# Optimization experiments

Hardware: AMD Instinct MI355X
Metric: run time of the kernel (lower is better)

Reference implementation:

```python
import jax, jax.numpy as jnp
import numpy as np

N = 100_000          # number of nodes
E = 3_200_000        # number of edges (avg degree 32)
IN_CH = 128
OUT_CH = 128


def setup_inputs() -> dict:
    key = jax.random.key(0)
    k1, k2, k3, k4 = jax.random.split(key, 4)
    x = jax.random.normal(k1, (N, IN_CH), dtype=jnp.float32)
    edge_index = jax.random.randint(k2, (2, E), 0, N, dtype=jnp.int32)
    # torch nn.Linear weights have shape [out_features, in_features]
    W_theta = jax.random.normal(k3, (OUT_CH, IN_CH), dtype=jnp.float32) / np.sqrt(IN_CH).astype(np.float32)
    W_phi = jax.random.normal(k4, (OUT_CH, OUT_CH), dtype=jnp.float32) / np.sqrt(OUT_CH).astype(np.float32)
    return {"x": x, "edge_index": edge_index, "W_theta": W_theta, "W_phi": W_phi}


def reference(x, edge_index, W_theta, W_phi):
    row, col = edge_index[0], edge_index[1]
    rel_pos = x[row] - x[col]                       # [E, in]
    rel_t = rel_pos @ W_theta.T                     # [E, out]
    aggr = jax.ops.segment_max(rel_t, row, num_segments=N)  # [N, out], -inf for empty segments
    # torch_scatter.scatter_max leaves empty segments at 0
    aggr = jnp.where(jnp.isneginf(aggr), jnp.zeros((), dtype=aggr.dtype), aggr)
    return aggr @ W_phi.T                           # [N, out]
```

## Files before the change

### kernel.cpp

```cpp
#include <hip/hip_runtime.h>
#include <stdint.h>

#define N_NODES 100000
#define N_EDGES 3200000
#define CH 128
#define NBUK 391
#define CAP 8704
#define SPLITB 782
#define EPB 4096
#define ROWS_A 50048

typedef __bf16 bf16x8 __attribute__((ext_vector_type(8)));
typedef float  floatx4 __attribute__((ext_vector_type(4)));

__device__ __forceinline__ unsigned short f2bf_bits(float f) {
    unsigned u = __float_as_uint(f);
    u += 0x7FFFu + ((u >> 16) & 1u);
    return (unsigned short)(u >> 16);
}

__device__ __forceinline__ unsigned short enc16(unsigned short b) {
    return b ^ ((b & 0x8000u) ? 0xFFFFu : 0x8000u);
}

__device__ __forceinline__ unsigned pkminu(unsigned a, unsigned b) {
    unsigned d;
    asm("v_pk_min_u16 %0, %1, %2" : "=v"(d) : "v"(a), "v"(b));
    return d;
}

__device__ __forceinline__ unsigned dec2(unsigned k) {
    unsigned lo = k & 0xFFFFu;
    unsigned hi = k >> 16;
    lo ^= (lo & 0x8000u) ? 0x8000u : 0xFFFFu;
    hi ^= (hi & 0x8000u) ? 0x8000u : 0xFFFFu;
    return lo | (hi << 16);
}

__device__ __forceinline__ bf16x8 pack8(floatx4 f0, floatx4 f1) {
    bf16x8 r;
    r[0] = (__bf16)f0[0]; r[1] = (__bf16)f0[1]; r[2] = (__bf16)f0[2]; r[3] = (__bf16)f0[3];
    r[4] = (__bf16)f1[0]; r[5] = (__bf16)f1[1]; r[6] = (__bf16)f1[2]; r[7] = (__bf16)f1[3];
    return r;
}

__device__ __forceinline__ void gemm_tile(int row0, int lane, const float* __restrict__ x,
                                          const unsigned short* __restrict__ wb,
                                          unsigned short* __restrict__ yt) {
    int m = lane & 15, quad = lane >> 4;
    bf16x8 a[4];
    const floatx4* xp = (const floatx4*)(x + (size_t)(row0 + m) * CH + quad * 8);
#pragma unroll
    for (int ks = 0; ks < 4; ks++) a[ks] = pack8(xp[ks * 8], xp[ks * 8 + 1]);

    for (int nt = 0; nt < 8; nt++) {
        const bf16x8* wp = (const bf16x8*)(wb + (size_t)(nt * 16 + m) * CH + quad * 8);
        floatx4 acc = {0.f, 0.f, 0.f, 0.f};
#pragma unroll
        for (int ks = 0; ks < 4; ks++)
            acc = __builtin_amdgcn_mfma_f32_16x16x32_bf16(a[ks], wp[ks * 4], acc, 0, 0, 0);
#pragma unroll
        for (int r = 0; r < 4; r++) {
            int orow = row0 + quad * 4 + r;
            yt[(size_t)orow * CH + nt * 16 + m] = enc16(f2bf_bits(acc[r]));
        }
    }
}

__global__ void k_setup(const float* __restrict__ Wt, const float* __restrict__ Wp,
                        unsigned short* __restrict__ wb, int* __restrict__ cursor) {
    int bid = blockIdx.x, t = threadIdx.x;
    if (bid < 128) {
        int i = bid * 256 + t;
        float v = (i < 16384) ? Wt[i] : Wp[i - 16384];
        wb[i] = f2bf_bits(v);
    } else {
        for (int i = t; i < NBUK; i += 256) cursor[i] = i * CAP;
    }
}

__global__ void k_split_gemmyA(const int* __restrict__ row, const int* __restrict__ col,
                               int* __restrict__ cursor, unsigned* __restrict__ pairs,
                               const float* __restrict__ x,
                               const unsigned short* __restrict__ wb,
                               unsigned short* __restrict__ yt) {
    __shared__ unsigned lpair[EPB];
    __shared__ int h[NBUK];
    __shared__ int hb[NBUK];
    __shared__ int lbase[NBUK];
    __shared__ int cur[NBUK];
    __shared__ int sc[512];
    int bid = blockIdx.x, t = threadIdx.x;
    if (bid < SPLITB) {
        for (int i = t; i < NBUK; i += 256) h[i] = 0;
        __syncthreads();
        int e0 = bid * EPB;
        int4 r[4];
        bool v[4];
#pragma unroll
        for (int j = 0; j < 4; j++) {
            int idx = e0 + j * 1024 + t * 4;
            v[j] = idx < N_EDGES;
            if (v[j]) {
                r[j] = *(const int4*)(row + idx);
                atomicAdd(&h[r[j].x >> 8], 1);
                atomicAdd(&h[r[j].y >> 8], 1);
                atomicAdd(&h[r[j].z >> 8], 1);
                atomicAdd(&h[r[j].w >> 8], 1);
            }
        }
        __syncthreads();
        for (int i = t; i < NBUK; i += 256) {
            int c = h[i];
            hb[i] = c ? atomicAdd(&cursor[i], c) : 0;
        }
        sc[t] = h[t];
        sc[t + 256] = (t + 256 < NBUK) ? h[t + 256] : 0;
        __syncthreads();
        for (int off = 1; off < 512; off <<= 1) {
            int a0 = (t >= off) ? sc[t - off] : 0;
            int a1 = (t + 256 >= off) ? sc[t + 256 - off] : 0;
            __syncthreads();
            sc[t] += a0;
            sc[t + 256] += a1;
            __syncthreads();
        }
        for (int i = t; i < NBUK; i += 256) {
            int lb = sc[i] - h[i];
            lbase[i] = lb;
            cur[i] = lb;
        }
        __syncthreads();
#pragma unroll
        for (int j = 0; j < 4; j++) {
            if (v[j]) {
                int idx = e0 + j * 1024 + t * 4;
                int4 c = *(const int4*)(col + idx);
                int b, p;
                b = r[j].x >> 8; p = atomicAdd(&cur[b], 1);
                lpair[p] = ((unsigned)(r[j].x & 255) << 17) | (unsigned)c.x;
                b = r[j].y >> 8; p = atomicAdd(&cur[b], 1);
                lpair[p] = ((unsigned)(r[j].y & 255) << 17) | (unsigned)c.y;
                b = r[j].z >> 8; p = atomicAdd(&cur[b], 1);
                lpair[p] = ((unsigned)(r[j].z & 255) << 17) | (unsigned)c.z;
                b = r[j].w >> 8; p = atomicAdd(&cur[b], 1);
                lpair[p] = ((unsigned)(r[j].w & 255) << 17) | (unsigned)c.w;
            }
        }
        __syncthreads();
        for (int b = t; b < NBUK; b += 256) {
            int n = h[b];
            if (!n) continue;
            int src = lbase[b];
            int dst = hb[b];
            int lim = (b + 1) * CAP - dst;
            if (n > lim) n = lim;
            for (int k = 0; k < n; k++) pairs[dst + k] = lpair[src + k];
        }
    } else {
        int wave = (bid - SPLITB) * 4 + (t >> 6);
        int row0 = wave * 16;
        if (row0 >= ROWS_A) return;
        gemm_tile(row0, t & 63, x, wb, yt);
    }
}

__global__ void k_build_gemmyB(unsigned* __restrict__ pairs, const int* __restrict__ cursor,
                               int* __restrict__ deg, int* __restrict__ offs,
                               const float* __restrict__ x,
                               const unsigned short* __restrict__ wb,
                               unsigned short* __restrict__ yt) {
    __shared__ int hist[256];
    __shared__ int sc[256];
    __shared__ int cur[256];
    __shared__ int lcsr[CAP];
    int bid = blockIdx.x, t = threadIdx.x;
    if (bid < NBUK) {
        int b = bid;
        int s0 = b * CAP;
        int cnt = cursor[b] - s0;
        if (cnt > CAP) cnt = CAP;
        if (t < 256) hist[t] = 0;
        __syncthreads();
        for (int i = t; i < cnt; i += 1024) {
            unsigned p = pairs[s0 + i];
            atomicAdd(&hist[p >> 17], 1);
        }
        __syncthreads();
        int d = 0;
        if (t < 256) { d = hist[t]; sc[t] = d; }
        __syncthreads();
        for (int off = 1; off < 256; off <<= 1) {
            int vv = 0;
            if (t < 256 && t >= off) vv = sc[t - off];
            __syncthreads();
            if (t < 256) sc[t] += vv;
            __syncthreads();
        }
        if (t < 256) {
            int excl = sc[t] - d;
            int node = b * 256 + t;
            if (node < N_NODES) {
                deg[node] = d;
                offs[node] = s0 + excl;
            }
            cur[t] = excl;
        }
        __syncthreads();
        for (int i = t; i < cnt; i += 1024) {
            unsigned p = pairs[s0 + i];
            int pos = atomicAdd(&cur[p >> 17], 1);
            lcsr[pos] = (int)(p & 0x1FFFFu);
        }
        __syncthreads();
        int* csr = (int*)pairs;
        for (int i = t; i < cnt; i += 1024) csr[s0 + i] = lcsr[i];
    } else {
        int wg = (bid - NBUK) * 16 + (t >> 6);
        int row0 = ROWS_A + wg * 16;
        if (row0 >= N_NODES) return;
        gemm_tile(row0, t & 63, x, wb, yt);
    }
}

#define PKA(v)                        \
    do {                              \
        m0 = pkminu(m0, (v).x);       \
        m1 = pkminu(m1, (v).y);       \
        m2 = pkminu(m2, (v).z);       \
        m3 = pkminu(m3, (v).w);       \
    } while (0)

__global__ void k_minaggr_out(const uint4* __restrict__ yt, const int* __restrict__ offs,
                              const int* __restrict__ deg, const int* __restrict__ csr,
                              const unsigned short* __restrict__ wb,
                              float* __restrict__ out) {
    __shared__ unsigned short atile[16 * 136];
    int t = threadIdx.x;
    int wave = t >> 6, lane = t & 63;
    int q = lane >> 4, s = lane & 15;
    int nl = wave * 4 + q;
    int n = blockIdx.x * 16 + nl;

    int i = offs[n];
    int len = deg[n];
    int end = i + len;

    unsigned m0 = ~0u, m1 = ~0u, m2 = ~0u, m3 = ~0u;

    for (; i + 8 <= end; i += 8) {
        int c0 = csr[i + 0];
        int c1 = csr[i + 1];
        int c2 = csr[i + 2];
        int c3 = csr[i + 3];
        int c4 = csr[i + 4];
        int c5 = csr[i + 5];
        int c6 = csr[i + 6];
        int c7 = csr[i + 7];
        uint4 v0 = yt[(size_t)c0 * 16 + s];
        uint4 v1 = yt[(size_t)c1 * 16 + s];
        uint4 v2 = yt[(size_t)c2 * 16 + s];
        uint4 v3 = yt[(size_t)c3 * 16 + s];
        uint4 v4 = yt[(size_t)c4 * 16 + s];
        uint4 v5 = yt[(size_t)c5 * 16 + s];
        uint4 v6 = yt[(size_t)c6 * 16 + s];
        uint4 v7 = yt[(size_t)c7 * 16 + s];
        PKA(v0); PKA(v1); PKA(v2); PKA(v3);
        PKA(v4); PKA(v5); PKA(v6); PKA(v7);
    }
    for (; i < end; i++) {
        int c = csr[i];
        uint4 v = yt[(size_t)c * 16 + s];
        PKA(v);
    }

    uint4 outv = {0u, 0u, 0u, 0u};
    if (len > 0) {
        unsigned d0 = dec2(m0), d1 = dec2(m1), d2 = dec2(m2), d3 = dec2(m3);
        uint4 se = yt[(size_t)n * 16 + s];
        unsigned s0 = dec2(se.x), s1 = dec2(se.y), s2 = dec2(se.z), s3 = dec2(se.w);
        outv.x = (unsigned)f2bf_bits(__uint_as_float(s0 << 16) - __uint_as_float(d0 << 16)) |
                 ((unsigned)f2bf_bits(__uint_as_float(s0 & 0xFFFF0000u) -
                                      __uint_as_float(d0 & 0xFFFF0000u)) << 16);
        outv.y = (unsigned)f2bf_bits(__uint_as_float(s1 << 16) - __uint_as_float(d1 << 16)) |
                 ((unsigned)f2bf_bits(__uint_as_float(s1 & 0xFFFF0000u) -
                                      __uint_as_float(d1 & 0xFFFF0000u)) << 16);
        outv.z = (unsigned)f2bf_bits(__uint_as_float(s2 << 16) - __uint_as_float(d2 << 16)) |
                 ((unsigned)f2bf_bits(__uint_as_float(s2 & 0xFFFF0000u) -
                                      __uint_as_float(d2 & 0xFFFF0000u)) << 16);
        outv.w = (unsigned)f2bf_bits(__uint_as_float(s3 << 16) - __uint_as_float(d3 << 16)) |
                 ((unsigned)f2bf_bits(__uint_as_float(s3 & 0xFFFF0000u) -
                                      __uint_as_float(d3 & 0xFFFF0000u)) << 16);
    }
    *(uint4*)&atile[nl * 136 + s * 8] = outv;
    __syncthreads();

    int m = lane & 15, quad = lane >> 4;
    bf16x8 a[4];
#pragma unroll
    for (int ks = 0; ks < 4; ks++)
        a[ks] = *(const bf16x8*)&atile[m * 136 + ks * 32 + quad * 8];

#pragma unroll
    for (int ntl = 0; ntl < 2; ntl++) {
        int nt = wave * 2 + ntl;
        const bf16x8* wp = (const bf16x8*)(wb + (size_t)(nt * 16 + m) * CH + quad * 8);
        floatx4 acc = {0.f, 0.f, 0.f, 0.f};
#pragma unroll
        for (int ks = 0; ks < 4; ks++)
            acc = __builtin_amdgcn_mfma_f32_16x16x32_bf16(a[ks], wp[ks * 4], acc, 0, 0, 0);
#pragma unroll
        for (int r = 0; r < 4; r++)
            out[(size_t)(blockIdx.x * 16 + quad * 4 + r) * CH + nt * 16 + m] = acc[r];
    }
}

extern "C" void kernel_launch(void* const* d_in, const int* in_sizes, int n_in,
                              void* d_out, int out_size, void* d_ws, size_t ws_size,
                              hipStream_t stream) {
    const float* x   = (const float*)d_in[0];
    const int* edge  = (const int*)d_in[1];
    const float* Wt  = (const float*)d_in[2];
    const float* Wp  = (const float*)d_in[3];
    const int* row = edge;
    const int* col = edge + N_EDGES;
    float* out = (float*)d_out;

    char* ws = (char*)d_ws;
    int* deg    = (int*)ws;  ws += 400128;
    int* offs   = (int*)ws;  ws += 400128;
    int* cursor = (int*)ws;  ws += 2048;
    unsigned short* yt = (unsigned short*)ws; ws += 25600000;
    unsigned short* wb = (unsigned short*)ws; ws += 65536;
    unsigned* pairs = (unsigned*)ws; ws += (size_t)NBUK * CAP * 4;

    k_setup<<<129, 256, 0, stream>>>(Wt, Wp, wb, cursor);
    k_split_gemmyA<<<SPLITB + 782, 256, 0, stream>>>(row, col, cursor, pairs,
                                                     x, wb, yt);
    k_build_gemmyB<<<NBUK + 196, 1024, 0, stream>>>(pairs, cursor, deg, offs, x, wb, yt);
    k_minaggr_out<<<N_NODES / 16, 256, 0, stream>>>((const uint4*)yt, offs, deg,
                                                    (const int*)pairs, wb + 16384, out);
}
```

Before: 296.1 us.

## Replace atomic bucket cursors with deterministic histogram-scan-scatter and spread GEMM over stages

Bucket partitioning now runs in three kernels instead of one fused split kernel with global atomics. A per-block histogram is written out, a per-bucket scan across blocks computes deterministic base offsets, and a scatter pass re-reads row and col to place the pairs. The dense x·Wθ GEMM tiles are spread evenly across the four pre-aggregation kernels so they fill the otherwise light stages. This removes the global atomic contention on cursor and makes bucket ordering deterministic, at the cost of an extra launch, a second read of row, and about 2.4 MB of counts/bases traffic.

```diff
diff --git a/kernel.cpp b/kernel.cpp
--- a/kernel.cpp
+++ b/kernel.cpp
@@ -8,7 +8,6 @@
 #define CAP 8704
 #define SPLITB 782
 #define EPB 4096
-#define ROWS_A 50048
 
 typedef __bf16 bf16x8 __attribute__((ext_vector_type(8)));
 typedef float  floatx4 __attribute__((ext_vector_type(4)));
@@ -68,22 +67,93 @@
 }
 
 __global__ void k_setup(const float* __restrict__ Wt, const float* __restrict__ Wp,
-                        unsigned short* __restrict__ wb, int* __restrict__ cursor) {
+                        unsigned short* __restrict__ wb) {
+    int i = blockIdx.x * 256 + threadIdx.x;
+    float v = (i < 16384) ? Wt[i] : Wp[i - 16384];
+    wb[i] = f2bf_bits(v);
+}
+
+__global__ void k_hist_gemmy(const int* __restrict__ row, int* __restrict__ counts,
+                             const float* __restrict__ x,
+                             const unsigned short* __restrict__ wb,
+                             unsigned short* __restrict__ yt) {
+    __shared__ int h[NBUK];
     int bid = blockIdx.x, t = threadIdx.x;
-    if (bid < 128) {
-        int i = bid * 256 + t;
-        float v = (i < 16384) ? Wt[i] : Wp[i - 16384];
-        wb[i] = f2bf_bits(v);
+    if (bid < SPLITB) {
+        for (int i = t; i < NBUK; i += 256) h[i] = 0;
+        __syncthreads();
+        int e0 = bid * EPB;
+#pragma unroll
+        for (int j = 0; j < 4; j++) {
+            int idx = e0 + j * 1024 + t * 4;
+            if (idx < N_EDGES) {
+                int4 r = *(const int4*)(row + idx);
+                atomicAdd(&h[r.x >> 8], 1);
+                atomicAdd(&h[r.y >> 8], 1);
+                atomicAdd(&h[r.z >> 8], 1);
+                atomicAdd(&h[r.w >> 8], 1);
+            }
+        }
+        __syncthreads();
+        for (int i = t; i < NBUK; i += 256) counts[bid * NBUK + i] = h[i];
     } else {
-        for (int i = t; i < NBUK; i += 256) cursor[i] = i * CAP;
-    }
-}
-
-__global__ void k_split_gemmyA(const int* __restrict__ row, const int* __restrict__ col,
-                               int* __restrict__ cursor, unsigned* __restrict__ pairs,
-                               const float* __restrict__ x,
-                               const unsigned short* __restrict__ wb,
-                               unsigned short* __restrict__ yt) {
+        int wave = (bid - SPLITB) * 4 + (t >> 6);
+        int row0 = wave * 16;
+        if (row0 >= 25024) return;
+        gemm_tile(row0, t & 63, x, wb, yt);
+    }
+}
+
+__global__ void k_scan_gemmy(const int* __restrict__ counts, int* __restrict__ bases,
+                             int* __restrict__ bcnt,
+                             const float* __restrict__ x,
+                             const unsigned short* __restrict__ wb,
+                             unsigned short* __restrict__ yt) {
+    __shared__ int sc[256];
+    int bid = blockIdx.x, t = threadIdx.x;
+    if (bid < NBUK) {
+        int b = bid;
+        int v[4];
+        int s = 0;
+#pragma unroll
+        for (int k = 0; k < 4; k++) {
+            int blk = t * 4 + k;
+            v[k] = (blk < SPLITB) ? counts[blk * NBUK + b] : 0;
+            s += v[k];
+        }
+        sc[t] = s;
+        __syncthreads();
+        for (int off = 1; off < 256; off <<= 1) {
+            int a = (t >= off) ? sc[t - off] : 0;
+            __syncthreads();
+            sc[t] += a;
+            __syncthreads();
+        }
+        int incl = sc[t];
+        int run = incl - s;
+#pragma unroll
+        for (int k = 0; k < 4; k++) {
+            int blk = t * 4 + k;
+            if (blk < SPLITB) {
+                bases[blk * NBUK + b] = b * CAP + run;
+                run += v[k];
+            }
+        }
+        if (t == 255) bcnt[b] = incl;
+    } else {
+        int wave = (bid - NBUK) * 4 + (t >> 6);
+        int row0 = 25024 + wave * 16;
+        if (row0 >= 50048) return;
+        gemm_tile(row0, t & 63, x, wb, yt);
+    }
+}
+
+__global__ void k_scatter_gemmy(const int* __restrict__ row, const int* __restrict__ col,
+                                const int* __restrict__ counts, const int* __restrict__ bases,
+                                unsigned* __restrict__ pairs,
+                                const float* __restrict__ x,
+                                const unsigned short* __restrict__ wb,
+                                unsigned short* __restrict__ yt) {
     __shared__ unsigned lpair[EPB];
     __shared__ int h[NBUK];
     __shared__ int hb[NBUK];
@@ -92,27 +162,9 @@
     __shared__ int sc[512];
     int bid = blockIdx.x, t = threadIdx.x;
     if (bid < SPLITB) {
-        for (int i = t; i < NBUK; i += 256) h[i] = 0;
-        __syncthreads();
-        int e0 = bid * EPB;
-        int4 r[4];
-        bool v[4];
-#pragma unroll
-        for (int j = 0; j < 4; j++) {
-            int idx = e0 + j * 1024 + t * 4;
-            v[j] = idx < N_EDGES;
-            if (v[j]) {
-                r[j] = *(const int4*)(row + idx);
-                atomicAdd(&h[r[j].x >> 8], 1);
-                atomicAdd(&h[r[j].y >> 8], 1);
-                atomicAdd(&h[r[j].z >> 8], 1);
-                atomicAdd(&h[r[j].w >> 8], 1);
-            }
-        }
-        __syncthreads();
         for (int i = t; i < NBUK; i += 256) {
-            int c = h[i];
-            hb[i] = c ? atomicAdd(&cursor[i], c) : 0;
+            h[i] = counts[bid * NBUK + i];
+            hb[i] = bases[bid * NBUK + i];
         }
         sc[t] = h[t];
         sc[t + 256] = (t + 256 < NBUK) ? h[t + 256] : 0;
@@ -131,20 +183,22 @@
             cur[i] = lb;
         }
         __syncthreads();
+        int e0 = bid * EPB;
 #pragma unroll
         for (int j = 0; j < 4; j++) {
-            if (v[j]) {
-                int idx = e0 + j * 1024 + t * 4;
+            int idx = e0 + j * 1024 + t * 4;
+            if (idx < N_EDGES) {
+                int4 r = *(const int4*)(row + idx);
                 int4 c = *(const int4*)(col + idx);
                 int b, p;
-                b = r[j].x >> 8; p = atomicAdd(&cur[b], 1);
-                lpair[p] = ((unsigned)(r[j].x & 255) << 17) | (unsigned)c.x;
-                b = r[j].y >> 8; p = atomicAdd(&cur[b], 1);
-                lpair[p] = ((unsigned)(r[j].y & 255) << 17) | (unsigned)c.y;
-                b = r[j].z >> 8; p = atomicAdd(&cur[b], 1);
-                lpair[p] = ((unsigned)(r[j].z & 255) << 17) | (unsigned)c.z;
-                b = r[j].w >> 8; p = atomicAdd(&cur[b], 1);
-                lpair[p] = ((unsigned)(r[j].w & 255) << 17) | (unsigned)c.w;
+                b = r.x >> 8; p = atomicAdd(&cur[b], 1);
+                lpair[p] = ((unsigned)(r.x & 255) << 17) | (unsigned)c.x;
+                b = r.y >> 8; p = atomicAdd(&cur[b], 1);
+                lpair[p] = ((unsigned)(r.y & 255) << 17) | (unsigned)c.y;
+                b = r.z >> 8; p = atomicAdd(&cur[b], 1);
+                lpair[p] = ((unsigned)(r.z & 255) << 17) | (unsigned)c.z;
+                b = r.w >> 8; p = atomicAdd(&cur[b], 1);
+                lpair[p] = ((unsigned)(r.w & 255) << 17) | (unsigned)c.w;
             }
         }
         __syncthreads();
@@ -159,17 +213,17 @@
         }
     } else {
         int wave = (bid - SPLITB) * 4 + (t >> 6);
-        int row0 = wave * 16;
-        if (row0 >= ROWS_A) return;
+        int row0 = 50048 + wave * 16;
+        if (row0 >= 75072) return;
         gemm_tile(row0, t & 63, x, wb, yt);
     }
 }
 
-__global__ void k_build_gemmyB(unsigned* __restrict__ pairs, const int* __restrict__ cursor,
-                               int* __restrict__ deg, int* __restrict__ offs,
-                               const float* __restrict__ x,
-                               const unsigned short* __restrict__ wb,
-                               unsigned short* __restrict__ yt) {
+__global__ void k_build_gemmy(unsigned* __restrict__ pairs, const int* __restrict__ bcnt,
+                              int* __restrict__ deg, int* __restrict__ offs,
+                              const float* __restrict__ x,
+                              const unsigned short* __restrict__ wb,
+                              unsigned short* __restrict__ yt) {
     __shared__ int hist[256];
     __shared__ int sc[256];
     __shared__ int cur[256];
@@ -178,7 +232,7 @@
     if (bid < NBUK) {
         int b = bid;
         int s0 = b * CAP;
-        int cnt = cursor[b] - s0;
+        int cnt = bcnt[b];
         if (cnt > CAP) cnt = CAP;
         if (t < 256) hist[t] = 0;
         __syncthreads();
@@ -217,7 +271,7 @@
         for (int i = t; i < cnt; i += 1024) csr[s0 + i] = lcsr[i];
     } else {
         int wg = (bid - NBUK) * 16 + (t >> 6);
-        int row0 = ROWS_A + wg * 16;
+        int row0 = 75072 + wg * 16;
         if (row0 >= N_NODES) return;
         gemm_tile(row0, t & 63, x, wb, yt);
     }
@@ -329,15 +383,19 @@
     char* ws = (char*)d_ws;
     int* deg    = (int*)ws;  ws += 400128;
     int* offs   = (int*)ws;  ws += 400128;
-    int* cursor = (int*)ws;  ws += 2048;
+    int* bcnt   = (int*)ws;  ws += 2048;
+    int* counts = (int*)ws;  ws += 1223168;
+    int* bases  = (int*)ws;  ws += 1223168;
     unsigned short* yt = (unsigned short*)ws; ws += 25600000;
     unsigned short* wb = (unsigned short*)ws; ws += 65536;
     unsigned* pairs = (unsigned*)ws; ws += (size_t)NBUK * CAP * 4;
 
-    k_setup<<<129, 256, 0, stream>>>(Wt, Wp, wb, cursor);
-    k_split_gemmyA<<<SPLITB + 782, 256, 0, stream>>>(row, col, cursor, pairs,
-                                                     x, wb, yt);
-    k_build_gemmyB<<<NBUK + 196, 1024, 0, stream>>>(pairs, cursor, deg, offs, x, wb, yt);
+    k_setup<<<128, 256, 0, stream>>>(Wt, Wp, wb);
+    k_hist_gemmy<<<SPLITB + 391, 256, 0, stream>>>(row, counts, x, wb, yt);
+    k_scan_gemmy<<<NBUK + 391, 256, 0, stream>>>(counts, bases, bcnt, x, wb, yt);
+    k_scatter_gemmy<<<SPLITB + 391, 256, 0, stream>>>(row, col, counts, bases, pairs,
+                                                      x, wb, yt);
+    k_build_gemmy<<<NBUK + 98, 1024, 0, stream>>>(pairs, bcnt, deg, offs, x, wb, yt);
     k_minaggr_out<<<N_NODES / 16, 256, 0, stream>>>((const uint4*)yt, offs, deg,
                                                     (const int*)pairs, wb + 16384, out);
 }
```

Result: no change. 294.2 us (-0.6%).

## Split yt into two channel banks and gather-min each half in separate kernels

Applied to the files above, without the earlier changes.

Stores the projected node features as two 64-channel banks instead of one 128-channel row layout. The min-aggregation then runs as two passes, each gathering only one bank, so each pass has a 12.8 MB working set that may stay resident in cache. The first half-result goes through an intermediate buffer, and the second kernel adds the output GEMM over 32 nodes per block. The cost is an extra launch, a second read of the CSR indices, and an extra write and read of the intermediate buffer.

```diff
diff --git a/kernel.cpp b/kernel.cpp
--- a/kernel.cpp
+++ b/kernel.cpp
@@ -9,6 +9,7 @@
 #define SPLITB 782
 #define EPB 4096
 #define ROWS_A 50048
+#define BANK_U4 800000
 
 typedef __bf16 bf16x8 __attribute__((ext_vector_type(8)));
 typedef float  floatx4 __attribute__((ext_vector_type(4)));
@@ -62,7 +63,8 @@
 #pragma unroll
         for (int r = 0; r < 4; r++) {
             int orow = row0 + quad * 4 + r;
-            yt[(size_t)orow * CH + nt * 16 + m] = enc16(f2bf_bits(acc[r]));
+            yt[(size_t)(nt >> 2) * (N_NODES * 64) + (size_t)orow * 64 + (nt & 3) * 16 + m] =
+                enc16(f2bf_bits(acc[r]));
         }
     }
 }
@@ -231,79 +233,118 @@
         m3 = pkminu(m3, (v).w);       \
     } while (0)
 
-__global__ void k_minaggr_out(const uint4* __restrict__ yt, const int* __restrict__ offs,
-                              const int* __restrict__ deg, const int* __restrict__ csr,
-                              const unsigned short* __restrict__ wb,
-                              float* __restrict__ out) {
-    __shared__ unsigned short atile[16 * 136];
+__device__ __forceinline__ uint4 finish_half(unsigned m0, unsigned m1, unsigned m2, unsigned m3,
+                                             uint4 se) {
+    unsigned d0 = dec2(m0), d1 = dec2(m1), d2 = dec2(m2), d3 = dec2(m3);
+    unsigned s0 = dec2(se.x), s1 = dec2(se.y), s2 = dec2(se.z), s3 = dec2(se.w);
+    uint4 o;
+    o.x = (unsigned)f2bf_bits(__uint_as_float(s0 << 16) - __uint_as_float(d0 << 16)) |
+          ((unsigned)f2bf_bits(__uint_as_float(s0 & 0xFFFF0000u) -
+                               __uint_as_float(d0 & 0xFFFF0000u)) << 16);
+    o.y = (unsigned)f2bf_bits(__uint_as_float(s1 << 16) - __uint_as_float(d1 << 16)) |
+          ((unsigned)f2bf_bits(__uint_as_float(s1 & 0xFFFF0000u) -
+                               __uint_as_float(d1 & 0xFFFF0000u)) << 16);
+    o.z = (unsigned)f2bf_bits(__uint_as_float(s2 << 16) - __uint_as_float(d2 << 16)) |
+          ((unsigned)f2bf_bits(__uint_as_float(s2 & 0xFFFF0000u) -
+                               __uint_as_float(d2 & 0xFFFF0000u)) << 16);
+    o.w = (unsigned)f2bf_bits(__uint_as_float(s3 << 16) - __uint_as_float(d3 << 16)) |
+          ((unsigned)f2bf_bits(__uint_as_float(s3 & 0xFFFF0000u) -
+                               __uint_as_float(d3 & 0xFFFF0000u)) << 16);
+    return o;
+}
+
+__global__ void k_min0(const uint4* __restrict__ yt, const int* __restrict__ offs,
+                       const int* __restrict__ deg, const int* __restrict__ csr,
+                       uint4* __restrict__ mbuf) {
     int t = threadIdx.x;
-    int wave = t >> 6, lane = t & 63;
-    int q = lane >> 4, s = lane & 15;
-    int nl = wave * 4 + q;
-    int n = blockIdx.x * 16 + nl;
+    int lane = t & 63;
+    int nl = (t >> 6) * 8 + (lane >> 3);
+    int s8 = lane & 7;
+    int n = blockIdx.x * 32 + nl;
 
     int i = offs[n];
     int len = deg[n];
     int end = i + len;
-
     unsigned m0 = ~0u, m1 = ~0u, m2 = ~0u, m3 = ~0u;
 
     for (; i + 8 <= end; i += 8) {
-        int c0 = csr[i + 0];
-        int c1 = csr[i + 1];
-        int c2 = csr[i + 2];
-        int c3 = csr[i + 3];
-        int c4 = csr[i + 4];
-        int c5 = csr[i + 5];
-        int c6 = csr[i + 6];
-        int c7 = csr[i + 7];
-        uint4 v0 = yt[(size_t)c0 * 16 + s];
-        uint4 v1 = yt[(size_t)c1 * 16 + s];
-        uint4 v2 = yt[(size_t)c2 * 16 + s];
-        uint4 v3 = yt[(size_t)c3 * 16 + s];
-        uint4 v4 = yt[(size_t)c4 * 16 + s];
-        uint4 v5 = yt[(size_t)c5 * 16 + s];
-        uint4 v6 = yt[(size_t)c6 * 16 + s];
-        uint4 v7 = yt[(size_t)c7 * 16 + s];
+        int c0 = csr[i + 0], c1 = csr[i + 1], c2 = csr[i + 2], c3 = csr[i + 3];
+        int c4 = csr[i + 4], c5 = csr[i + 5], c6 = csr[i + 6], c7 = csr[i + 7];
+        uint4 v0 = yt[(size_t)c0 * 8 + s8];
+        uint4 v1 = yt[(size_t)c1 * 8 + s8];
+        uint4 v2 = yt[(size_t)c2 * 8 + s8];
+        uint4 v3 = yt[(size_t)c3 * 8 + s8];
+        uint4 v4 = yt[(size_t)c4 * 8 + s8];
+        uint4 v5 = yt[(size_t)c5 * 8 + s8];
+        uint4 v6 = yt[(size_t)c6 * 8 + s8];
+        uint4 v7 = yt[(size_t)c7 * 8 + s8];
         PKA(v0); PKA(v1); PKA(v2); PKA(v3);
         PKA(v4); PKA(v5); PKA(v6); PKA(v7);
     }
     for (; i < end; i++) {
-        int c = csr[i];
-        uint4 v = yt[(size_t)c * 16 + s];
+        uint4 v = yt[(size_t)csr[i] * 8 + s8];
         PKA(v);
     }
 
     uint4 outv = {0u, 0u, 0u, 0u};
-    if (len > 0) {
-        unsigned d0 = dec2(m0), d1 = dec2(m1), d2 = dec2(m2), d3 = dec2(m3);
-        uint4 se = yt[(size_t)n * 16 + s];
-        unsigned s0 = dec2(se.x), s1 = dec2(se.y), s2 = dec2(se.z), s3 = dec2(se.w);
-        outv.x = (unsigned)f2bf_bits(__uint_as_float(s0 << 16) - __uint_as_float(d0 << 16)) |
-                 ((unsigned)f2bf_bits(__uint_as_float(s0 & 0xFFFF0000u) -
-                                      __uint_as_float(d0 & 0xFFFF0000u)) << 16);
-        outv.y = (unsigned)f2bf_bits(__uint_as_float(s1 << 16) - __uint_as_float(d1 << 16)) |
-                 ((unsigned)f2bf_bits(__uint_as_float(s1 & 0xFFFF0000u) -
-                                      __uint_as_float(d1 & 0xFFFF0000u)) << 16);
-        outv.z = (unsigned)f2bf_bits(__uint_as_float(s2 << 16) - __uint_as_float(d2 << 16)) |
-                 ((unsigned)f2bf_bits(__uint_as_float(s2 & 0xFFFF0000u) -
-                                      __uint_as_float(d2 & 0xFFFF0000u)) << 16);
-        outv.w = (unsigned)f2bf_bits(__uint_as_float(s3 << 16) - __uint_as_float(d3 << 16)) |
-                 ((unsigned)f2bf_bits(__uint_as_float(s3 & 0xFFFF0000u) -
-                                      __uint_as_float(d3 & 0xFFFF0000u)) << 16);
-    }
-    *(uint4*)&atile[nl * 136 + s * 8] = outv;
+    if (len > 0) outv = finish_half(m0, m1, m2, m3, yt[(size_t)n * 8 + s8]);
+    mbuf[(size_t)n * 8 + s8] = outv;
+}
+
+__global__ void k_min1_out(const uint4* __restrict__ yt, const int* __restrict__ offs,
+                           const int* __restrict__ deg, const int* __restrict__ csr,
+                           const uint4* __restrict__ mbuf,
+                           const unsigned short* __restrict__ wb,
+                           float* __restrict__ out) {
+    __shared__ unsigned short atile[32 * 136];
+    int t = threadIdx.x;
+    int wave = t >> 6, lane = t & 63;
+    int nl = wave * 8 + (lane >> 3);
+    int s8 = lane & 7;
+    int n = blockIdx.x * 32 + nl;
+    const uint4* yt1 = yt + BANK_U4;
+
+    int i = offs[n];
+    int len = deg[n];
+    int end = i + len;
+    unsigned m0 = ~0u, m1 = ~0u, m2 = ~0u, m3 = ~0u;
+
+    for (; i + 8 <= end; i += 8) {
+        int c0 = csr[i + 0], c1 = csr[i + 1], c2 = csr[i + 2], c3 = csr[i + 3];
+        int c4 = csr[i + 4], c5 = csr[i + 5], c6 = csr[i + 6], c7 = csr[i + 7];
+        uint4 v0 = yt1[(size_t)c0 * 8 + s8];
+        uint4 v1 = yt1[(size_t)c1 * 8 + s8];
+        uint4 v2 = yt1[(size_t)c2 * 8 + s8];
+        uint4 v3 = yt1[(size_t)c3 * 8 + s8];
+        uint4 v4 = yt1[(size_t)c4 * 8 + s8];
+        uint4 v5 = yt1[(size_t)c5 * 8 + s8];
+        uint4 v6 = yt1[(size_t)c6 * 8 + s8];
+        uint4 v7 = yt1[(size_t)c7 * 8 + s8];
+        PKA(v0); PKA(v1); PKA(v2); PKA(v3);
+        PKA(v4); PKA(v5); PKA(v6); PKA(v7);
+    }
+    for (; i < end; i++) {
+        uint4 v = yt1[(size_t)csr[i] * 8 + s8];
+        PKA(v);
+    }
+
+    uint4 outv = {0u, 0u, 0u, 0u};
+    if (len > 0) outv = finish_half(m0, m1, m2, m3, yt1[(size_t)n * 8 + s8]);
+    *(uint4*)&atile[nl * 136 + 64 + s8 * 8] = outv;
+    *(uint4*)&atile[nl * 136 + s8 * 8] = mbuf[(size_t)n * 8 + s8];
     __syncthreads();
 
     int m = lane & 15, quad = lane >> 4;
+    int mt = wave & 1;
+    int ng = wave >> 1;
     bf16x8 a[4];
 #pragma unroll
     for (int ks = 0; ks < 4; ks++)
-        a[ks] = *(const bf16x8*)&atile[m * 136 + ks * 32 + quad * 8];
-
-#pragma unroll
-    for (int ntl = 0; ntl < 2; ntl++) {
-        int nt = wave * 2 + ntl;
+        a[ks] = *(const bf16x8*)&atile[(mt * 16 + m) * 136 + ks * 32 + quad * 8];
+
+#pragma unroll
+    for (int ntl = 0; ntl < 4; ntl++) {
+        int nt = ng * 4 + ntl;
         const bf16x8* wp = (const bf16x8*)(wb + (size_t)(nt * 16 + m) * CH + quad * 8);
         floatx4 acc = {0.f, 0.f, 0.f, 0.f};
 #pragma unroll
@@ -311,7 +352,7 @@
             acc = __builtin_amdgcn_mfma_f32_16x16x32_bf16(a[ks], wp[ks * 4], acc, 0, 0, 0);
 #pragma unroll
         for (int r = 0; r < 4; r++)
-            out[(size_t)(blockIdx.x * 16 + quad * 4 + r) * CH + nt * 16 + m] = acc[r];
+            out[(size_t)(blockIdx.x * 32 + mt * 16 + quad * 4 + r) * CH + nt * 16 + m] = acc[r];
     }
 }
 
@@ -332,12 +373,14 @@
     int* cursor = (int*)ws;  ws += 2048;
     unsigned short* yt = (unsigned short*)ws; ws += 25600000;
     unsigned short* wb = (unsigned short*)ws; ws += 65536;
-    unsigned* pairs = (unsigned*)ws; ws += (size_t)NBUK * CAP * 4;
+    unsigned* pairs = (unsigned*)ws; ws += 13613056;
+    uint4* mbuf = (uint4*)ws; ws += 12800000;
 
     k_setup<<<129, 256, 0, stream>>>(Wt, Wp, wb, cursor);
-    k_split_gemmyA<<<SPLITB + 782, 256, 0, stream>>>(row, col, cursor, pairs,
-                                                     x, wb, yt);
+    k_split_gemmyA<<<SPLITB + 782, 256, 0, stream>>>(row, col, cursor, pairs, x, wb, yt);
     k_build_gemmyB<<<NBUK + 196, 1024, 0, stream>>>(pairs, cursor, deg, offs, x, wb, yt);
-    k_minaggr_out<<<N_NODES / 16, 256, 0, stream>>>((const uint4*)yt, offs, deg,
-                                                    (const int*)pairs, wb + 16384, out);
-}
+    k_min0<<<N_NODES / 32, 256, 0, stream>>>((const uint4*)yt, offs, deg,
+                                             (const int*)pairs, mbuf);
+    k_min1_out<<<N_NODES / 32, 256, 0, stream>>>((const uint4*)yt, offs, deg,
+                                                 (const int*)pairs, mbuf, wb + 16384, out);
+}
```

Result: no change. 300.6 us (+1.5%).
